# Kernel optimization log

Measured on AMD Instinct MI355X. Metric: run time of the kernel, lower is better.

## Reference

```python
import jax, jax.numpy as jnp
import numpy as np

B = 2
NCLS = 19    # semantic classes for the logits heads
NLAB = 20    # raw point label values 0..19 (0 = unlabeled)
# (Z, Y, X) grids at strides 2, 4, 8 of sizes=[256,256,32]
GRIDS = {2: (16, 128, 128), 4: (8, 64, 64), 8: (4, 32, 32)}


def _lin_idx(coord, Z, Y, X):
    # coord: (N,4) int rows [b, z, y, x] -> flat cell index over B*Z*Y*X
    b, z, y, x = coord[:, 0], coord[:, 1], coord[:, 2], coord[:, 3]
    return ((b * Z + z) * Y + y) * X + x


def _bev_projection(feat, coord, Y, X):
    # Fused equivalent of torch.unique + scatter_max + spconv dense():
    # scatter_max features directly into the dense (B, Y, X) BEV grid keyed by (b,y,x).
    key = (coord[:, 0] * Y + coord[:, 2]) * X + coord[:, 3]
    C = feat.shape[1]
    dense = jax.ops.segment_max(feat, key, num_segments=B * Y * X)  # empty cells -> -inf
    dense = jnp.where(jnp.isfinite(dense), dense, jnp.zeros((), feat.dtype))
    return dense.reshape(B, Y, X, C).transpose(0, 3, 1, 2)  # (B, C, Y, X)


def _voxel_sem_target(fcoord, pcoord, plabel, Z, Y, X):
    # Majority-vote semantic label per point voxel, gathered at feature voxel coords.
    ncell = B * Z * Y * X
    pair = _lin_idx(pcoord, Z, Y, X) * NLAB + plabel  # (cell, label) key
    counts = jax.ops.segment_sum(
        jnp.ones(pcoord.shape[0], jnp.int32), pair, num_segments=ncell * NLAB
    ).reshape(ncell, NLAB)
    maj = jnp.argmax(counts, axis=1).astype(jnp.int32)   # most frequent label per cell
    occ = counts.sum(axis=1) > 0                          # cell contains any point
    fk = _lin_idx(fcoord, Z, Y, X)
    return jnp.where(occ[fk], maj[fk], 0).astype(jnp.int32)  # unmatched -> 0


def _head(x, w1, g, b, w2, b2):
    # Linear(no bias) -> BatchNorm1d(train stats) -> LeakyReLU(0.1) -> Linear
    h = x @ w1
    mu = h.mean(axis=0)
    var = h.var(axis=0)
    h = (h - mu) * jax.lax.rsqrt(var + 1e-5) * g + b
    h = jnp.where(h >= 0, h, 0.1 * h)
    return h @ w2 + b2


def _rand_coords(key, n, Z, Y, X):
    kb, kz, ky, kx = jax.random.split(key, 4)
    return jnp.stack([
        jax.random.randint(kb, (n,), 0, B, dtype=jnp.int32),
        jax.random.randint(kz, (n,), 0, Z, dtype=jnp.int32),
        jax.random.randint(ky, (n,), 0, Y, dtype=jnp.int32),
        jax.random.randint(kx, (n,), 0, X, dtype=jnp.int32),
    ], axis=1)


def setup_inputs() -> dict:
    key = jax.random.key(0)
    ks = jax.random.split(key, 32)
    M1, M2, M3, NP = 200000, 100000, 50000, 500000
    inp = {
        'proj1_vw': jax.random.normal(ks[0], (M1, 64), jnp.float32),
        'proj2_vw': jax.random.normal(ks[1], (M2, 128), jnp.float32),
        'proj3_vw': jax.random.normal(ks[2], (M3, 256), jnp.float32),
        'vw1_coord': _rand_coords(ks[3], M1, *GRIDS[2]),
        'vw2_coord': _rand_coords(ks[4], M2, *GRIDS[4]),
        'vw3_coord': _rand_coords(ks[5], M3, *GRIDS[8]),
        'idx02': _rand_coords(ks[6], NP, *GRIDS[2]),
        'idx04': _rand_coords(ks[7], NP, *GRIDS[4]),
        'idx08': _rand_coords(ks[8], NP, *GRIDS[8]),
        'pw_label': jax.random.randint(ks[9], (NP,), 0, NLAB, dtype=jnp.int32),
    }
    # learned head parameters (out2 / out4 / out8)
    def head_params(k, cin):
        k1, k2 = jax.random.split(k)
        return (jax.random.normal(k1, (cin, 64), jnp.float32) * 0.02,
                jnp.ones((64,), jnp.float32), jnp.zeros((64,), jnp.float32),
                jax.random.normal(k2, (64, NCLS), jnp.float32) * 0.02,
                jnp.zeros((NCLS,), jnp.float32))
    for tag, k, cin in (('h2', ks[10], 64), ('h4', ks[11], 128), ('h8', ks[12], 256)):
        w1, g, b, w2, b2 = head_params(k, cin)
        inp[f'{tag}_w1'], inp[f'{tag}_g'], inp[f'{tag}_b'] = w1, g, b
        inp[f'{tag}_w2'], inp[f'{tag}_b2'] = w2, b2
    return inp


def reference(proj1_vw, proj2_vw, proj3_vw, vw1_coord, vw2_coord, vw3_coord,
              idx02, idx04, idx08, pw_label,
              h2_w1, h2_g, h2_b, h2_w2, h2_b2,
              h4_w1, h4_g, h4_b, h4_w2, h4_b2,
              h8_w1, h8_g, h8_b, h8_w2, h8_b2):
    (Z2, Y2, X2), (Z4, Y4, X4), (Z8, Y8, X8) = GRIDS[2], GRIDS[4], GRIDS[8]
    bev1 = _bev_projection(proj1_vw, vw1_coord, Y2, X2)   # (B, 64, 128, 128)
    bev2 = _bev_projection(proj2_vw, vw2_coord, Y4, X4)   # (B, 128, 64, 64)
    bev3 = _bev_projection(proj3_vw, vw3_coord, Y8, X8)   # (B, 256, 32, 32)
    lbl2 = _voxel_sem_target(vw1_coord, idx02, pw_label, Z2, Y2, X2)
    lbl4 = _voxel_sem_target(vw2_coord, idx04, pw_label, Z4, Y4, X4)
    lbl8 = _voxel_sem_target(vw3_coord, idx08, pw_label, Z8, Y8, X8)
    log2 = _head(proj1_vw, h2_w1, h2_g, h2_b, h2_w2, h2_b2)
    log4 = _head(proj2_vw, h4_w1, h4_g, h4_b, h4_w2, h4_b2)
    log8 = _head(proj3_vw, h8_w1, h8_g, h8_b, h8_w2, h8_b2)
    return (bev1, bev2, bev3, log2, log4, log8, lbl2, lbl4, lbl8)
```

## Files before the change

### kernel.cpp

```cpp
#include <hip/hip_runtime.h>
#include <hip/hip_bf16.h>

typedef unsigned int u32;
typedef unsigned short u16;
typedef __attribute__((ext_vector_type(8))) short short8;
typedef __attribute__((ext_vector_type(4))) float f32x4;

#define NLAB 20

#define M_1 200000
#define C_1 64
#define Z_1 16
#define Y_1 128
#define X_1 128

#define M_2 100000
#define C_2 128
#define Z_2 8
#define Y_2 64
#define X_2 64

#define M_3 50000
#define C_3 256
#define Z_3 4
#define Y_3 32
#define X_3 32

#define O_BEV1 0
#define O_BEV2 2097152
#define O_BEV3 3145728
#define O_LOG1 3670016
#define O_LOG2 7470016
#define O_LOG3 9370016
#define O_LBL1 10320016
#define O_LBL2 10520016
#define O_LBL3 10620016

#define NCELLS 43008
#define SB1 0
#define SB2 32768
#define SB3 40960

#define CAP1 40
#define CAP2 64
#define CAP3 96
#define P1 43008
#define P2 1353728
#define P3 1878016

#define WPART 2080000
#define WP1 0
#define WP2 400000
#define WP3 600064
#define WSTATS 2780160

#define WBEV_F  4194304
#define WBEV2_F 6291456
#define WBEV3_F 7340032

#define WC1_W 8388608
#define WC2_W 11010048
#define WC3_W 11337728
#define W_COUNT_BYTES 11960320ull
#define NZB 730

#define WH_BIG_U16 22806528
#define WH1 0
#define WH2 12800000
#define WH3 19200000

#define GB1 3125
#define GB2 1563
#define GB3 782
#define HB1 782
#define HB2 391
#define HB3 196
#define NHB (HB1 + HB2 + HB3)

#define NGEMM 5470
#define NGATH 3584
#define NCNT  5862
#define CH 128
#define NMEGA (117 * CH)

#define NTLH (29 * CH)

static __device__ __forceinline__ u16 f2bf(float f) {
  u32 u = __float_as_uint(f);
  u32 r = u + 0x7fffu + ((u >> 16) & 1u);
  return (u16)(r >> 16);
}


static __device__ __forceinline__ void dev_count(int cb, int tid,
    const int* i2, const int* i4, const int* i8, const int* lab, u32* hist)
{
  const int* pc; int Z, Y, X; u32* base; int i;
  if (cb < 1954)      { pc = i2; Z = Z_1; Y = Y_1; X = X_1; base = hist + WC1_W; i = cb * 256 + tid; }
  else if (cb < 3908) { pc = i4; Z = Z_2; Y = Y_2; X = X_2; base = hist + WC2_W; i = (cb - 1954) * 256 + tid; }
  else                { pc = i8; Z = Z_3; Y = Y_3; X = X_3; base = hist + WC3_W; i = (cb - 3908) * 256 + tid; }
  if (i >= 500000) return;
  int4 c = *(const int4*)(pc + i * 4);
  int l = lab[i];
  int lin = ((c.x * Z + c.y) * Y + c.z) * X + c.w;
  atomicAdd(base + lin * 5 + (l >> 2), 1u << ((l & 3) * 8));
}

#define GBATCH 8
static __device__ __forceinline__ void dev_gather(int gb, int tid,
    const float* f1, const float* f2, const float* f3,
    const int* cur2, const int* pidx2, float* ws)
{
  int w = gb * 4 + (tid >> 6);
  int lane = tid & 63;
  int t0 = w * 4;
  int C = (t0 < 32768) ? 64 : (t0 < 49152) ? 128 : 256;
  const float* fp[4]; int n[4], st[4]; u32 wb[4];
#pragma unroll
  for (int k = 0; k < 4; k++) {
    int t = t0 + k; const float* f; int cidx, stv, cap; u32 wbv;
    if (t < 32768) {
      f = f1; cidx = SB1 + t; stv = P1 + t * CAP1; cap = CAP1;
      wbv = WBEV_F + (u32)t * 64;
    } else if (t < 49152) {
      int u = t - 32768; int cell = u >> 1, ch = (u & 1) * 64;
      f = f2 + ch; cidx = SB2 + cell; stv = P2 + cell * CAP2; cap = CAP2;
      wbv = WBEV2_F + (u32)cell * 128 + ch;
    } else {
      int u = t - 49152; int cell = u >> 2, ch = (u & 3) * 64;
      f = f3 + ch; cidx = SB3 + cell; stv = P3 + cell * CAP3; cap = CAP3;
      wbv = WBEV3_F + (u32)cell * 256 + ch;
    }
    fp[k] = f; wb[k] = wbv; st[k] = stv;
    int cnt = cur2[cidx];
    n[k] = cnt < cap ? cnt : cap;
  }
  int maxn = max(max(n[0], n[1]), max(n[2], n[3]));
  float acc[4];
#pragma unroll
  for (int k = 0; k < 4; k++) acc[k] = __uint_as_float(0xff800000u);
  for (int base = 0; base < maxn; base += GBATCH) {
    int p[4][GBATCH];
#pragma unroll
    for (int k = 0; k < 4; k++) {
      int hi = st[k] + (n[k] > 0 ? n[k] - 1 : 0);
      int s = st[k] + base;
#pragma unroll
      for (int j = 0; j < GBATCH; j++) {
        int idx = s + j;
        idx = idx < hi ? idx : hi;
        int pv = pidx2[idx];
        p[k][j] = n[k] > 0 ? pv : 0;
      }
    }
    float v[4][GBATCH];
#pragma unroll
    for (int k = 0; k < 4; k++)
#pragma unroll
      for (int j = 0; j < GBATCH; j++)
        v[k][j] = fp[k][(size_t)p[k][j] * C + lane];
#pragma unroll
    for (int k = 0; k < 4; k++)
#pragma unroll
      for (int j = 0; j < GBATCH; j++)
        acc[k] = fmaxf(acc[k], v[k][j]);
  }
#pragma unroll
  for (int k = 0; k < 4; k++)
    ws[wb[k] + lane] = (n[k] > 0) ? acc[k] : 0.f;
}

static __device__ __forceinline__ void dev_gemm(int blk, int tid,
    const float* x1, const float* x2, const float* x3,
    const float* w1a, const float* w1b, const float* w1c,
    u16* hbuf, float* part)
{
  const float* x; const float* w1; u16* h; float* pp; int Cin, M, bl, NB;
  if (blk < GB1)            { x = x1; w1 = w1a; h = hbuf + WH1; pp = part + WP1; Cin = C_1; M = M_1; bl = blk;             NB = GB1; }
  else if (blk < GB1 + GB2) { x = x2; w1 = w1b; h = hbuf + WH2; pp = part + WP2; Cin = C_2; M = M_2; bl = blk - GB1;       NB = GB2; }
  else                      { x = x3; w1 = w1c; h = hbuf + WH3; pp = part + WP3; Cin = C_3; M = M_3; bl = blk - GB1 - GB2; NB = GB3; }
  int lane = tid & 63, wv = tid >> 6;
  int m16 = lane & 15, quad = lane >> 4;

  __shared__ u16 As[64 * 72];
  __shared__ u16 Bs[64 * 72];
  __shared__ float redS[4][64];
  __shared__ float redQ[4][64];

  f32x4 acc[4];
#pragma unroll
  for (int nt = 0; nt < 4; nt++) acc[nt] = (f32x4){0.f, 0.f, 0.f, 0.f};

  int nchunk = Cin >> 6;
  for (int c = 0; c < nchunk; c++) {
    if (c) __syncthreads();
#pragma unroll
    for (int pass = 0; pass < 4; pass++) {
      int fidx = pass * 256 + tid;
      int row = fidx >> 4, kp = (fidx & 15) * 4;
      int grow = bl * 64 + row;
      float4 v = make_float4(0.f, 0.f, 0.f, 0.f);
      if (grow < M) v = *(const float4*)(x + (size_t)grow * Cin + c * 64 + kp);
      ushort4 o = { f2bf(v.x), f2bf(v.y), f2bf(v.z), f2bf(v.w) };
      *(ushort4*)(As + row * 72 + kp) = o;
    }
    {
      int n = tid & 63, kg = tid >> 6;
#pragma unroll
      for (int p = 0; p < 4; p++) {
        int k0 = kg * 4 + p * 16;
        const float* wp = w1 + (size_t)(c * 64 + k0) * 64 + n;
        ushort4 o = { f2bf(wp[0]), f2bf(wp[64]), f2bf(wp[128]), f2bf(wp[192]) };
        *(ushort4*)(Bs + n * 72 + k0) = o;
      }
    }
    __syncthreads();
#pragma unroll
    for (int ks = 0; ks < 2; ks++) {
      short8 a0 = *(const short8*)(As + (wv * 16 + m16) * 72 + ks * 32 + quad * 8);
      short8 b[4];
#pragma unroll
      for (int nt = 0; nt < 4; nt++)
        b[nt] = *(const short8*)(Bs + (nt * 16 + m16) * 72 + ks * 32 + quad * 8);
#pragma unroll
      for (int nt = 0; nt < 4; nt++)
        acc[nt] = __builtin_amdgcn_mfma_f32_16x16x32_bf16(a0, b[nt], acc[nt], 0, 0, 0);
    }
  }

  float s[4] = {0.f, 0.f, 0.f, 0.f}, q[4] = {0.f, 0.f, 0.f, 0.f};
#pragma unroll
  for (int nt = 0; nt < 4; nt++) {
#pragma unroll
    for (int r = 0; r < 4; r++) {
      float v = acc[nt][r];
      int grow = bl * 64 + wv * 16 + quad * 4 + r;
      if (grow < M) h[(size_t)grow * 64 + nt * 16 + m16] = f2bf(v);
      s[nt] += v;
      q[nt] = fmaf(v, v, q[nt]);
    }
  }
#pragma unroll
  for (int nt = 0; nt < 4; nt++) {
    s[nt] += __shfl_xor(s[nt], 16); s[nt] += __shfl_xor(s[nt], 32);
    q[nt] += __shfl_xor(q[nt], 16); q[nt] += __shfl_xor(q[nt], 32);
  }
  if (lane < 16) {
#pragma unroll
    for (int nt = 0; nt < 4; nt++) {
      redS[wv][nt * 16 + lane] = s[nt];
      redQ[wv][nt * 16 + lane] = q[nt];
    }
  }
  __syncthreads();
  if (tid < 64) {
    pp[tid * NB + bl] = redS[0][tid] + redS[1][tid] + redS[2][tid] + redS[3][tid];
  } else if (tid < 128) {
    int n2 = tid - 64;
    pp[(64 + n2) * NB + bl] = redQ[0][n2] + redQ[1][n2] + redQ[2][n2] + redQ[3][n2];
  }
}

static __device__ __forceinline__ void dev_lbl(int blk, int tid,
    const int* fc1, const int* fc2, const int* fc3, const u32* hist, float* out)
{
  const int* fc; int Z, Y, X, M; const u32* base; long lbase; int m;
  if (blk < HB1)            { fc = fc1; Z = Z_1; Y = Y_1; X = X_1; M = M_1; base = hist + WC1_W; lbase = O_LBL1; m = blk * 256 + tid; }
  else if (blk < HB1 + HB2) { fc = fc2; Z = Z_2; Y = Y_2; X = X_2; M = M_2; base = hist + WC2_W; lbase = O_LBL2; m = (blk - HB1) * 256 + tid; }
  else                      { fc = fc3; Z = Z_3; Y = Y_3; X = X_3; M = M_3; base = hist + WC3_W; lbase = O_LBL3; m = (blk - HB1 - HB2) * 256 + tid; }
  if (m >= M) return;
  int4 c = *(const int4*)(fc + m * 4);
  int lin = ((c.x * Z + c.y) * Y + c.z) * X + c.w;
  const u32* cp = base + lin * 5;
  u32 w0 = cp[0], w1 = cp[1], w2 = cp[2], w3 = cp[3], w4 = cp[4];
  int best = (int)(w0 & 0xffu); int bi = 0;
#pragma unroll
  for (int n = 1; n < NLAB; n++) {
    u32 w = (n < 4) ? w0 : (n < 8) ? w1 : (n < 12) ? w2 : (n < 16) ? w3 : w4;
    int cc = (int)((w >> ((n & 3) * 8)) & 0xffu);
    if (cc > best) { best = cc; bi = n; }
  }
  out[lbase + m] = (float)bi;
}

static __device__ __forceinline__ void dev_transpose(int bid, int tid,
    const float* ws, float* out, float* tileU)
{
  if (bid < 512) {
    int b = bid >> 8, y = (bid >> 1) & 127, x0 = (bid & 1) * 64;
    const float* src = ws + WBEV_F + (size_t)((b * 128 + y) * 128 + x0) * 64;
#pragma unroll
    for (int pass = 0; pass < 16; pass++) {
      int idx = pass * 256 + tid;
      int x = idx >> 6, c = idx & 63;
      tileU[x * 65 + c] = src[(size_t)x * 64 + c];
    }
    __syncthreads();
    size_t ob = O_BEV1 + ((size_t)(b * 64) * 128 + y) * 128 + x0;
#pragma unroll
    for (int pass = 0; pass < 16; pass++) {
      int idx = pass * 256 + tid;
      int c = idx >> 6, x = idx & 63;
      out[ob + (size_t)c * 16384 + x] = tileU[x * 65 + c];
    }
  } else if (bid < 768) {
    int t = bid - 512;
    int b = t >> 7, y = (t >> 1) & 63, x0 = (t & 1) * 32;
    const float* src = ws + WBEV2_F + (size_t)((b * 64 + y) * 64 + x0) * 128;
#pragma unroll
    for (int pass = 0; pass < 16; pass++) {
      int idx = pass * 256 + tid;
      int x = idx >> 7, c = idx & 127;
      tileU[x * 129 + c] = src[(size_t)x * 128 + c];
    }
    __syncthreads();
    size_t ob = O_BEV2 + ((size_t)(b * 128) * 64 + y) * 64 + x0;
#pragma unroll
    for (int pass = 0; pass < 16; pass++) {
      int idx = pass * 256 + tid;
      int c = idx >> 5, x = idx & 31;
      out[ob + (size_t)c * 4096 + x] = tileU[x * 129 + c];
    }
  } else {
    int t = bid - 768;
    int b = t >> 6, y = (t >> 1) & 31, ch0 = (t & 1) * 128;
    const float* src = ws + WBEV3_F + (size_t)((b * 32 + y) * 32) * 256 + ch0;
#pragma unroll
    for (int pass = 0; pass < 16; pass++) {
      int idx = pass * 256 + tid;
      int x = idx >> 7, c = idx & 127;
      tileU[x * 129 + c] = src[(size_t)x * 256 + c];
    }
    __syncthreads();
    size_t ob = O_BEV3 + ((size_t)(b * 256 + ch0) * 32 + y) * 32;
#pragma unroll
    for (int pass = 0; pass < 16; pass++) {
      int idx = pass * 256 + tid;
      int c = idx >> 5, x = idx & 31;
      out[ob + (size_t)c * 1024 + x] = tileU[x * 129 + c];
    }
  }
}

static __device__ __forceinline__ void dev_stats(int sblk, int tid,
    const float* part, float* stats,
    const float* g1, const float* b1, const float* g4, const float* b4,
    const float* g8, const float* b8)
{
  int sc = sblk >> 6, col = sblk & 63;
  int nb; const float* p; float invM; const float* g; const float* bb;
  if (sc == 0)      { nb = GB1; p = part + WP1; invM = 1.f / M_1; g = g1; bb = b1; }
  else if (sc == 1) { nb = GB2; p = part + WP2; invM = 1.f / M_2; g = g4; bb = b4; }
  else              { nb = GB3; p = part + WP3; invM = 1.f / M_3; g = g8; bb = b8; }
  const float* ps = p + (size_t)col * nb;
  const float* pq = p + (size_t)(64 + col) * nb;
  float s = 0.f, q = 0.f;
  for (int i = tid; i < nb; i += 256) { s += ps[i]; q += pq[i]; }
  __shared__ float r1[256], r2[256];
  r1[tid] = s; r2[tid] = q;
  __syncthreads();
  for (int off = 128; off > 0; off >>= 1) {
    if (tid < off) { r1[tid] += r1[tid + off]; r2[tid] += r2[tid + off]; }
    __syncthreads();
  }
  if (tid == 0) {
    float mu  = r1[0] * invM;
    float var = r2[0] * invM - mu * mu;
    float scale = rsqrtf(var + 1e-5f) * g[col];
    stats[sc * 128 + col]      = scale;
    stats[sc * 128 + 64 + col] = fmaf(-mu, scale, bb[col]);
  }
}

static __device__ __forceinline__ void dev_head(int blk, int tid,
    const u16* hbuf, const float* stats,
    const float* w21, const float* c21, const float* w24, const float* c24,
    const float* w28, const float* c28, float* out, float* os)
{
  const u16* h; const float* st; const float* w2; const float* b2;
  int M; long obase; int bl;
  if (blk < HB1)            { h = hbuf + WH1; st = stats;       w2 = w21; b2 = c21; M = M_1; obase = O_LOG1; bl = blk; }
  else if (blk < HB1 + HB2) { h = hbuf + WH2; st = stats + 128; w2 = w24; b2 = c24; M = M_2; obase = O_LOG2; bl = blk - HB1; }
  else                      { h = hbuf + WH3; st = stats + 256; w2 = w28; b2 = c28; M = M_3; obase = O_LOG3; bl = blk - HB1 - HB2; }
  int rowbase = bl * 256;
  int avail = M - rowbase; if (avail > 256) avail = 256;

  float acc[19];
#pragma unroll
  for (int n = 0; n < 19; n++) acc[n] = 0.f;

  if (tid < avail) {
    const uint4* hr = (const uint4*)(h + (size_t)(rowbase + tid) * 64);
    uint4 d[8];
#pragma unroll
    for (int q = 0; q < 8; q++) d[q] = hr[q];
#pragma unroll
    for (int q = 0; q < 8; q++) {
#pragma unroll
      for (int half = 0; half < 2; half++) {
        u32 dx = half ? d[q].z : d[q].x;
        u32 dy = half ? d[q].w : d[q].y;
        int j = q * 8 + half * 4;
        float f0 = __uint_as_float(dx << 16);
        float f1 = __uint_as_float(dx & 0xffff0000u);
        float f2 = __uint_as_float(dy << 16);
        float f3 = __uint_as_float(dy & 0xffff0000u);
        float a0 = fmaf(f0, st[j],     st[64 + j]);     a0 = a0 >= 0.f ? a0 : 0.1f * a0;
        float a1 = fmaf(f1, st[j + 1], st[64 + j + 1]); a1 = a1 >= 0.f ? a1 : 0.1f * a1;
        float a2 = fmaf(f2, st[j + 2], st[64 + j + 2]); a2 = a2 >= 0.f ? a2 : 0.1f * a2;
        float a3 = fmaf(f3, st[j + 3], st[64 + j + 3]); a3 = a3 >= 0.f ? a3 : 0.1f * a3;
#pragma unroll
        for (int n = 0; n < 19; n++) {
          acc[n] = fmaf(a0, w2[j * 19 + n], acc[n]);
          acc[n] = fmaf(a1, w2[(j + 1) * 19 + n], acc[n]);
          acc[n] = fmaf(a2, w2[(j + 2) * 19 + n], acc[n]);
          acc[n] = fmaf(a3, w2[(j + 3) * 19 + n], acc[n]);
        }
      }
    }
#pragma unroll
    for (int n = 0; n < 19; n++) os[tid * 19 + n] = acc[n] + b2[n];
  }
  __syncthreads();
  int tot = avail * 19;
  float* op = out + obase + (size_t)rowbase * 19;
  for (int i = tid; i < tot; i += 256) op[i] = os[i];
}


__global__ __launch_bounds__(256) void k_scatter2(
    const int* __restrict__ co1, const int* __restrict__ co2, const int* __restrict__ co3,
    int* __restrict__ cur2, int* __restrict__ pidx2, uint4* __restrict__ histz)
{
  int blk = blockIdx.x;
  if (blk >= NHB) {
    int zb = blk - NHB;
    uint4 z = {0u, 0u, 0u, 0u};
    uint4* dst = histz + (size_t)zb * 1024 + threadIdx.x;
#pragma unroll
    for (int r = 0; r < 4; r++) dst[r * 256] = z;
    return;
  }
  const int* co; int Y, X, M, base, m, pbase, cap;
  if (blk < HB1)            { co = co1; Y = Y_1; X = X_1; M = M_1; base = SB1; pbase = P1; cap = CAP1; m = blk * 256 + threadIdx.x; }
  else if (blk < HB1 + HB2) { co = co2; Y = Y_2; X = X_2; M = M_2; base = SB2; pbase = P2; cap = CAP2; m = (blk - HB1) * 256 + threadIdx.x; }
  else                      { co = co3; Y = Y_3; X = X_3; M = M_3; base = SB3; pbase = P3; cap = CAP3; m = (blk - HB1 - HB2) * 256 + threadIdx.x; }
  if (m >= M) return;
  int4 c = *(const int4*)(co + m * 4);
  int cell = (c.x * Y + c.z) * X + c.w;
  int slot = atomicAdd(cur2 + base + cell, 1);
  if (slot < cap) pidx2[pbase + cell * cap + slot] = m;
}

__global__ __launch_bounds__(256) void k_mega(
    const float* __restrict__ x1, const float* __restrict__ x2, const float* __restrict__ x3,
    const float* __restrict__ w1a, const float* __restrict__ w1b, const float* __restrict__ w1c,
    u16* __restrict__ hbuf, float* __restrict__ part,
    const int* __restrict__ cur2, const int* __restrict__ pidx2,
    float* __restrict__ ws,
    const int* __restrict__ i2, const int* __restrict__ i4, const int* __restrict__ i8,
    const int* __restrict__ lab, u32* __restrict__ hist)
{
  int blk = blockIdx.x;
  int chunk = blk >> 7, off = blk & 127;
  int type, ci;
  if (chunk < 84)       { ci = chunk / 3;              type = chunk % 3; }
  else if (chunk < 114) { int j = chunk - 84; ci = 28 + (j >> 1); type = j & 1; }
  else                  { ci = 43 + (chunk - 114);     type = 1; }
  int idx = ci * CH + off;
  if (type == 0) {
    if (idx < NGEMM) dev_gemm(idx, threadIdx.x, x1, x2, x3, w1a, w1b, w1c, hbuf, part);
  } else if (type == 1) {
    if (idx < NCNT) dev_count(idx, threadIdx.x, i2, i4, i8, lab, hist);
  } else {
    if (idx < NGATH) dev_gather(idx, threadIdx.x, x1, x2, x3, cur2, pidx2, ws);
  }
}

__global__ __launch_bounds__(256) void k_stats(const float* __restrict__ part, float* __restrict__ stats,
    const float* __restrict__ g1, const float* __restrict__ b1,
    const float* __restrict__ g4, const float* __restrict__ b4,
    const float* __restrict__ g8, const float* __restrict__ b8)
{
  dev_stats(blockIdx.x, threadIdx.x, part, stats, g1, b1, g4, b4, g8, b8);
}

__global__ __launch_bounds__(256) void k_tlh(
    const u16* __restrict__ hbuf, const float* __restrict__ stats,
    const float* __restrict__ w21, const float* __restrict__ c21,
    const float* __restrict__ w24, const float* __restrict__ c24,
    const float* __restrict__ w28, const float* __restrict__ c28,
    const float* __restrict__ ws, const u32* __restrict__ hist,
    const int* __restrict__ fc1, const int* __restrict__ fc2, const int* __restrict__ fc3,
    float* __restrict__ out)
{
  __shared__ __align__(16) float smem[256 * 19];
  int blk = blockIdx.x;
  int chunk = blk >> 7, off = blk & 127;
  int type, ci;
  if (chunk < 21) { ci = chunk / 3;             type = chunk % 3; }
  else            { int j = chunk - 21; ci = 7 + (j >> 1); type = j & 1; }
  int idx = ci * CH + off;
  if (type == 0) {
    if (idx < NHB) dev_head(idx, threadIdx.x, hbuf, stats, w21, c21, w24, c24, w28, c28, out, smem);
  } else if (type == 1) {
    if (idx < NHB) dev_lbl(idx, threadIdx.x, fc1, fc2, fc3, hist, out);
  } else {
    if (idx < 896) dev_transpose(idx, threadIdx.x, ws, out, smem);
  }
}

extern "C" void kernel_launch(void* const* d_in, const int* in_sizes, int n_in,
                              void* d_out, int out_size, void* d_ws, size_t ws_size,
                              hipStream_t stream) {
  (void)in_sizes; (void)n_in; (void)out_size; (void)ws_size;
  const float* p1 = (const float*)d_in[0];
  const float* p2 = (const float*)d_in[1];
  const float* p3 = (const float*)d_in[2];
  const int* vc1  = (const int*)d_in[3];
  const int* vc2  = (const int*)d_in[4];
  const int* vc3  = (const int*)d_in[5];
  const int* i2   = (const int*)d_in[6];
  const int* i4   = (const int*)d_in[7];
  const int* i8   = (const int*)d_in[8];
  const int* lab  = (const int*)d_in[9];
  const float* h2w1 = (const float*)d_in[10]; const float* h2g = (const float*)d_in[11];
  const float* h2b  = (const float*)d_in[12]; const float* h2w2 = (const float*)d_in[13];
  const float* h2b2 = (const float*)d_in[14];
  const float* h4w1 = (const float*)d_in[15]; const float* h4g = (const float*)d_in[16];
  const float* h4b  = (const float*)d_in[17]; const float* h4w2 = (const float*)d_in[18];
  const float* h4b2 = (const float*)d_in[19];
  const float* h8w1 = (const float*)d_in[20]; const float* h8g = (const float*)d_in[21];
  const float* h8b  = (const float*)d_in[22]; const float* h8w2 = (const float*)d_in[23];
  const float* h8b2 = (const float*)d_in[24];

  float* out = (float*)d_out;
  int* wsi = (int*)d_ws;
  u32* wsu = (u32*)d_ws;
  float* wsf = (float*)d_ws;
  u16* wsh = (u16*)d_ws;

  u16* hbig = wsh + WH_BIG_U16;
  float* pbig = wsf + WPART;
  float* sbig = wsf + WSTATS;

  hipMemsetAsync(wsi, 0, NCELLS * sizeof(int), stream);

  k_scatter2<<<NHB + NZB, 256, 0, stream>>>(vc1, vc2, vc3, wsi, wsi,
      (uint4*)(wsu + WC1_W));

  k_mega<<<NMEGA, 256, 0, stream>>>(p1, p2, p3,
      h2w1, h4w1, h8w1, hbig, pbig,
      wsi, wsi, wsf,
      i2, i4, i8, lab, wsu);

  k_stats<<<192, 256, 0, stream>>>(pbig, sbig, h2g, h2b, h4g, h4b, h8g, h8b);

  k_tlh<<<NTLH, 256, 0, stream>>>(hbig, sbig,
      h2w2, h2b2, h4w2, h4b2, h8w2, h8b2,
      wsf, wsu, vc1, vc2, vc3, out);
}
```

Measured before the change: 396.2 us.

## Overlap scatter and histogram zeroing with first GEMM chunks in fused launch

New measurement: 388.1 us. 1.02x faster.

```diff
diff --git a/kernel.cpp b/kernel.cpp
--- a/kernel.cpp
+++ b/kernel.cpp
@@ -81,7 +81,13 @@
 #define NGATH 3584
 #define NCNT  5862
 #define CH 128
-#define NMEGA (117 * CH)
+
+#define SCH 17
+#define G1CH 20
+#define NSG ((SCH + G1CH) * CH)
+
+#define G2CH 23
+#define NMEGA2 ((69 + 28) * CH)
 
 #define NTLH (29 * CH)
 
@@ -104,6 +110,31 @@
   int l = lab[i];
   int lin = ((c.x * Z + c.y) * Y + c.z) * X + c.w;
   atomicAdd(base + lin * 5 + (l >> 2), 1u << ((l & 3) * 8));
+}
+
+static __device__ __forceinline__ void dev_scatter(int idx, int tid,
+    const int* co1, const int* co2, const int* co3,
+    int* cur2, int* pidx2, uint4* histz)
+{
+  if (idx >= NHB) {
+    int zb = idx - NHB;
+    if (zb < NZB) {
+      uint4 z = {0u, 0u, 0u, 0u};
+      uint4* dst = histz + (size_t)zb * 1024 + tid;
+#pragma unroll
+      for (int r = 0; r < 4; r++) dst[r * 256] = z;
+    }
+    return;
+  }
+  const int* co; int Y, X, M, base, m, pbase, cap;
+  if (idx < HB1)            { co = co1; Y = Y_1; X = X_1; M = M_1; base = SB1; pbase = P1; cap = CAP1; m = idx * 256 + tid; }
+  else if (idx < HB1 + HB2) { co = co2; Y = Y_2; X = X_2; M = M_2; base = SB2; pbase = P2; cap = CAP2; m = (idx - HB1) * 256 + tid; }
+  else                      { co = co3; Y = Y_3; X = X_3; M = M_3; base = SB3; pbase = P3; cap = CAP3; m = (idx - HB1 - HB2) * 256 + tid; }
+  if (m >= M) return;
+  int4 c = *(const int4*)(co + m * 4);
+  int cell = (c.x * Y + c.z) * X + c.w;
+  int slot = atomicAdd(cur2 + base + cell, 1);
+  if (slot < cap) pidx2[pbase + cell * cap + slot] = m;
 }
 
 #define GBATCH 8
@@ -428,31 +459,31 @@
 }
 
 
-__global__ __launch_bounds__(256) void k_scatter2(
+__global__ __launch_bounds__(256) void k_sg(
     const int* __restrict__ co1, const int* __restrict__ co2, const int* __restrict__ co3,
-    int* __restrict__ cur2, int* __restrict__ pidx2, uint4* __restrict__ histz)
+    int* __restrict__ cur2, int* __restrict__ pidx2, uint4* __restrict__ histz,
+    const float* __restrict__ x1, const float* __restrict__ x2, const float* __restrict__ x3,
+    const float* __restrict__ w1a, const float* __restrict__ w1b, const float* __restrict__ w1c,
+    u16* __restrict__ hbuf, float* __restrict__ part)
 {
   int blk = blockIdx.x;
-  if (blk >= NHB) {
-    int zb = blk - NHB;
-    uint4 z = {0u, 0u, 0u, 0u};
-    uint4* dst = histz + (size_t)zb * 1024 + threadIdx.x;
-#pragma unroll
-    for (int r = 0; r < 4; r++) dst[r * 256] = z;
-    return;
-  }
-  const int* co; int Y, X, M, base, m, pbase, cap;
-  if (blk < HB1)            { co = co1; Y = Y_1; X = X_1; M = M_1; base = SB1; pbase = P1; cap = CAP1; m = blk * 256 + threadIdx.x; }
-  else if (blk < HB1 + HB2) { co = co2; Y = Y_2; X = X_2; M = M_2; base = SB2; pbase = P2; cap = CAP2; m = (blk - HB1) * 256 + threadIdx.x; }
-  else                      { co = co3; Y = Y_3; X = X_3; M = M_3; base = SB3; pbase = P3; cap = CAP3; m = (blk - HB1 - HB2) * 256 + threadIdx.x; }
-  if (m >= M) return;
-  int4 c = *(const int4*)(co + m * 4);
-  int cell = (c.x * Y + c.z) * X + c.w;
-  int slot = atomicAdd(cur2 + base + cell, 1);
-  if (slot < cap) pidx2[pbase + cell * cap + slot] = m;
-}
-
-__global__ __launch_bounds__(256) void k_mega(
+  int chunk = blk >> 7, off = blk & 127;
+  if (chunk < 2 * SCH) {
+    int ci = chunk >> 1;
+    int idx = ci * CH + off;
+    if (chunk & 1) {
+      if (idx < NHB + NZB) dev_scatter(idx, threadIdx.x, co1, co2, co3, cur2, pidx2, histz);
+    } else {
+      dev_gemm(idx, threadIdx.x, x1, x2, x3, w1a, w1b, w1c, hbuf, part);
+    }
+  } else {
+    int ci = SCH + (chunk - 2 * SCH);
+    int idx = ci * CH + off;
+    dev_gemm(idx, threadIdx.x, x1, x2, x3, w1a, w1b, w1c, hbuf, part);
+  }
+}
+
+__global__ __launch_bounds__(256) void k_mega2(
     const float* __restrict__ x1, const float* __restrict__ x2, const float* __restrict__ x3,
     const float* __restrict__ w1a, const float* __restrict__ w1b, const float* __restrict__ w1c,
     u16* __restrict__ hbuf, float* __restrict__ part,
@@ -463,16 +494,17 @@
 {
   int blk = blockIdx.x;
   int chunk = blk >> 7, off = blk & 127;
-  int type, ci;
-  if (chunk < 84)       { ci = chunk / 3;              type = chunk % 3; }
-  else if (chunk < 114) { int j = chunk - 84; ci = 28 + (j >> 1); type = j & 1; }
-  else                  { ci = 43 + (chunk - 114);     type = 1; }
-  int idx = ci * CH + off;
-  if (type == 0) {
-    if (idx < NGEMM) dev_gemm(idx, threadIdx.x, x1, x2, x3, w1a, w1b, w1c, hbuf, part);
-  } else if (type == 1) {
-    if (idx < NCNT) dev_count(idx, threadIdx.x, i2, i4, i8, lab, hist);
+  if (chunk < 69) {
+    int tri = chunk / 3, t = chunk % 3;
+    if (t == 0) {
+      int idx = (G1CH + tri) * CH + off;
+      if (idx < NGEMM) dev_gemm(idx, threadIdx.x, x1, x2, x3, w1a, w1b, w1c, hbuf, part);
+    } else {
+      int idx = (tri * 2 + (t - 1)) * CH + off;
+      if (idx < NCNT) dev_count(idx, threadIdx.x, i2, i4, i8, lab, hist);
+    }
   } else {
+    int idx = (chunk - 69) * CH + off;
     if (idx < NGATH) dev_gather(idx, threadIdx.x, x1, x2, x3, cur2, pidx2, ws);
   }
 }
@@ -546,10 +578,10 @@
 
   hipMemsetAsync(wsi, 0, NCELLS * sizeof(int), stream);
 
-  k_scatter2<<<NHB + NZB, 256, 0, stream>>>(vc1, vc2, vc3, wsi, wsi,
-      (uint4*)(wsu + WC1_W));
-
-  k_mega<<<NMEGA, 256, 0, stream>>>(p1, p2, p3,
+  k_sg<<<NSG, 256, 0, stream>>>(vc1, vc2, vc3, wsi, wsi, (uint4*)(wsu + WC1_W),
+      p1, p2, p3, h2w1, h4w1, h8w1, hbig, pbig);
+
+  k_mega2<<<NMEGA2, 256, 0, stream>>>(p1, p2, p3,
       h2w1, h4w1, h8w1, hbig, pbig,
       wsi, wsi, wsf,
       i2, i4, i8, lab, wsu);
```
